# Performance work log

Hardware: AMD Instinct MI355X
Metric: run time of the kernel (lower is better)

## Reference

```python
import jax, jax.numpy as jnp
import numpy as np
import math

H = 1e-4  # finite-difference step
TW = math.pi / 8.0  # transition width
LOW = math.pi / 2.0 - TW
HIGH = math.pi / 2.0 + TW


def _smooth_step(t):
    # equivalent to torch smooth_step with masks: 0 below LOW, 1 above HIGH,
    x = jnp.clip((t - LOW) / (HIGH - LOW), 0.0, 1.0)
    return x * x * (3.0 - 2.0 * x)


def _compute_potential(xyz, a_param, b_param, direction):
    # xyz: [B,3]
    a = jnp.clip(a_param, 0.0, 20.0)
    b = jnp.clip(b_param, 0.0, 20.0)
    r2 = jnp.sum(xyz * xyz, axis=1)          # [B]
    r = jnp.sqrt(r2)
    origin = r == 0.0
    safe_r = jnp.where(origin, 1.0, r)
    p_hat = xyz / safe_r[:, None]            # [B,3]
    dot = p_hat @ direction                  # [B]
    theta = jnp.arccos(jnp.clip(dot, -1.0, 1.0))
    w = _smooth_step(theta)
    # w*direct + (1-w)*ray = 0.5*a*r^2 + (1-w)*0.5*b*r^2*theta^2
    pot = 0.5 * a * r2 + (1.0 - w) * 0.5 * b * r2 * theta * theta
    return jnp.where(origin, 0.0, pot)


def setup_inputs() -> dict:
    key = jax.random.key(0)
    B = 8388608
    xyz = jax.random.normal(key, (B, 3), dtype=jnp.float32)
    theta_dir, phi_dir = 1.0471975511965976, 0.7853981633974483
    direction = jnp.array([
        math.sin(theta_dir) * math.cos(phi_dir),
        math.sin(theta_dir) * math.sin(phi_dir),
        math.cos(theta_dir),
    ], dtype=jnp.float32)
    a_param = jnp.float32(1.0)
    b_param = jnp.float32(10.0)
    return {"xyz": xyz, "a_param": a_param, "b_param": b_param, "direction": direction}


def reference(xyz, a_param, b_param, direction):
    # compute_velocity: central finite differences of the potential, negated
    eye = jnp.eye(3, dtype=xyz.dtype)
    grads = []
    for i in range(3):  # fixed tiny loop over xyz axes
        u_plus = _compute_potential(xyz + H * eye[i], a_param, b_param, direction)
        u_minus = _compute_potential(xyz - H * eye[i], a_param, b_param, direction)
        grads.append((u_plus - u_minus) / (2.0 * H))
    velocity = -jnp.stack(grads, axis=1)  # [B,3]
    return velocity
```

## Files before the change

kernel.cpp:

```cpp
#include <hip/hip_runtime.h>
#include <math.h>

#define HF 1e-4f

#define LOW_F  1.1780972450961724f
#define INV_TW 1.2732395447351628f

__device__ __forceinline__ float fast_acos(float x) {
    float s = __builtin_fabsf(x);
    bool big = s > 0.5f;
    float z = big ? fmaf(-0.5f, s, 0.5f) : x * x;
    float r = big ? __builtin_amdgcn_sqrtf(z) : s;
    float p = fmaf(z, 4.2163199048e-2f, 2.4181311049e-2f);
    p = fmaf(z, p, 4.5470025998e-2f);
    p = fmaf(z, p, 7.4953002686e-2f);
    p = fmaf(z, p, 1.6666752422e-1f);
    float asn = fmaf(r * z, p, r);
    float t2 = 2.0f * asn;
    float rb = (x >= 0.0f) ? t2 : (3.14159274f - t2);
    float rs = (x >= 0.0f) ? (1.57079637f - asn) : (1.57079637f + asn);
    return big ? rb : rs;
}

__device__ __forceinline__ float pot_eval(float x, float y, float z,
                                          float halfa, float halfb,
                                          float dx, float dy, float dz) {
    float r2 = x * x + y * y + z * z;
    float r = __builtin_amdgcn_sqrtf(r2);
    float invr = __builtin_amdgcn_rcpf(r);
    float dot = (x * dx + y * dy + z * dz) * invr;
    dot = fminf(fmaxf(dot, -1.0f), 1.0f);
    float theta = fast_acos(dot);
    float t = (theta - LOW_F) * INV_TW;
    t = fminf(fmaxf(t, 0.0f), 1.0f);
    float w = t * t * (3.0f - 2.0f * t);
    float pot = halfa * r2 + (1.0f - w) * halfb * r2 * theta * theta;
    return (r2 == 0.0f) ? 0.0f : pot;
}

__device__ __forceinline__ void point_velocity(float x, float y, float z,
                                               float halfa, float halfb,
                                               float dx, float dy, float dz,
                                               float& vx, float& vy, float& vz) {
    const float inv2H = 1.0f / 2e-4f;
    float upx = pot_eval(x + HF, y, z, halfa, halfb, dx, dy, dz);
    float umx = pot_eval(x - HF, y, z, halfa, halfb, dx, dy, dz);
    float upy = pot_eval(x, y + HF, z, halfa, halfb, dx, dy, dz);
    float umy = pot_eval(x, y - HF, z, halfa, halfb, dx, dy, dz);
    float upz = pot_eval(x, y, z + HF, halfa, halfb, dx, dy, dz);
    float umz = pot_eval(x, y, z - HF, halfa, halfb, dx, dy, dz);
    vx = -(upx - umx) * inv2H;
    vy = -(upy - umy) * inv2H;
    vz = -(upz - umz) * inv2H;
}

extern "C" __global__ void __launch_bounds__(256)
canyon3d_fd_kernel(const float* __restrict__ xyz,
                   const float* __restrict__ a_param,
                   const float* __restrict__ b_param,
                   const float* __restrict__ dir,
                   float* __restrict__ out,
                   int B) {
    int t = blockIdx.x * blockDim.x + threadIdx.x;
    int base = t * 4;
    if (base >= B) return;

    float a = fminf(fmaxf(a_param[0], 0.0f), 20.0f);
    float b = fminf(fmaxf(b_param[0], 0.0f), 20.0f);
    float halfa = 0.5f * a;
    float halfb = 0.5f * b;
    float dx = dir[0], dy = dir[1], dz = dir[2];

    if (base + 4 <= B) {
        const float4* in4 = (const float4*)xyz;
        float4 A  = in4[3 * t + 0];
        float4 Bv = in4[3 * t + 1];
        float4 C  = in4[3 * t + 2];

        float o0, o1, o2, o3, o4, o5, o6, o7, o8, o9, o10, o11;
        point_velocity(A.x, A.y, A.z,  halfa, halfb, dx, dy, dz, o0, o1, o2);
        point_velocity(A.w, Bv.x, Bv.y, halfa, halfb, dx, dy, dz, o3, o4, o5);
        point_velocity(Bv.z, Bv.w, C.x, halfa, halfb, dx, dy, dz, o6, o7, o8);
        point_velocity(C.y, C.z, C.w,  halfa, halfb, dx, dy, dz, o9, o10, o11);

        float4* out4 = (float4*)out;
        out4[3 * t + 0] = make_float4(o0, o1, o2, o3);
        out4[3 * t + 1] = make_float4(o4, o5, o6, o7);
        out4[3 * t + 2] = make_float4(o8, o9, o10, o11);
    } else {
        for (int i = base; i < B; ++i) {
            float x = xyz[3 * i], y = xyz[3 * i + 1], z = xyz[3 * i + 2];
            float vx, vy, vz;
            point_velocity(x, y, z, halfa, halfb, dx, dy, dz, vx, vy, vz);
            out[3 * i] = vx; out[3 * i + 1] = vy; out[3 * i + 2] = vz;
        }
    }
}

extern "C" void kernel_launch(void* const* d_in, const int* in_sizes, int n_in,
                              void* d_out, int out_size, void* d_ws, size_t ws_size,
                              hipStream_t stream) {
    const float* xyz = (const float*)d_in[0];
    const float* a_param = (const float*)d_in[1];
    const float* b_param = (const float*)d_in[2];
    const float* dir = (const float*)d_in[3];
    float* out = (float*)d_out;

    int B = in_sizes[0] / 3;
    int nthreads = (B + 3) / 4;
    dim3 block(256);
    dim3 grid((nthreads + 255) / 256);
    canyon3d_fd_kernel<<<grid, block, 0, stream>>>(xyz, a_param, b_param, dir, out, B);
}
```

Before: 185.1 us.

## Replace finite-difference potential evaluations with closed-form analytic gradient

Computes the velocity as the exact analytic gradient of the potential instead of six central finite-difference evaluations per point. This removes five of six sqrt/rcp/acos evaluations per point, cutting ALU work so the kernel can approach the memory bound. The result differs slightly from the finite-difference reference, and a clamped reciprocal of sin(theta) guards the pole singularity, which risks accuracy mismatch near dot=±1.

```diff
diff --git a/kernel.cpp b/kernel.cpp
--- a/kernel.cpp
+++ b/kernel.cpp
@@ -1,10 +1,9 @@
 #include <hip/hip_runtime.h>
 #include <math.h>
 
-#define HF 1e-4f
-
-#define LOW_F  1.1780972450961724f
-#define INV_TW 1.2732395447351628f
+#define LOW_F   1.1780972450961724f
+#define INV_TW  1.2732395447351628f
+#define WP_K    7.639437268410977f
 
 __device__ __forceinline__ float fast_acos(float x) {
     float s = __builtin_fabsf(x);
@@ -22,53 +21,60 @@
     return big ? rb : rs;
 }
 
-__device__ __forceinline__ float pot_eval(float x, float y, float z,
-                                          float halfa, float halfb,
-                                          float dx, float dy, float dz) {
+__device__ __forceinline__ void point_velocity(float x, float y, float z,
+                                               float a, float b,
+                                               float dx, float dy, float dz,
+                                               float& vx, float& vy, float& vz) {
     float r2 = x * x + y * y + z * z;
     float r = __builtin_amdgcn_sqrtf(r2);
     float invr = __builtin_amdgcn_rcpf(r);
     float dot = (x * dx + y * dy + z * dz) * invr;
     dot = fminf(fmaxf(dot, -1.0f), 1.0f);
     float theta = fast_acos(dot);
+
     float t = (theta - LOW_F) * INV_TW;
     t = fminf(fmaxf(t, 0.0f), 1.0f);
     float w = t * t * (3.0f - 2.0f * t);
-    float pot = halfa * r2 + (1.0f - w) * halfb * r2 * theta * theta;
-    return (r2 == 0.0f) ? 0.0f : pot;
-}
+    float one_m_w = 1.0f - w;
+    float wp = WP_K * t * (1.0f - t);
 
-__device__ __forceinline__ void point_velocity(float x, float y, float z,
-                                               float halfa, float halfb,
-                                               float dx, float dy, float dz,
-                                               float& vx, float& vy, float& vz) {
-    const float inv2H = 1.0f / 2e-4f;
-    float upx = pot_eval(x + HF, y, z, halfa, halfb, dx, dy, dz);
-    float umx = pot_eval(x - HF, y, z, halfa, halfb, dx, dy, dz);
-    float upy = pot_eval(x, y + HF, z, halfa, halfb, dx, dy, dz);
-    float umy = pot_eval(x, y - HF, z, halfa, halfb, dx, dy, dz);
-    float upz = pot_eval(x, y, z + HF, halfa, halfb, dx, dy, dz);
-    float umz = pot_eval(x, y, z - HF, halfa, halfb, dx, dy, dz);
-    vx = -(upx - umx) * inv2H;
-    vy = -(upy - umy) * inv2H;
-    vz = -(upz - umz) * inv2H;
+    float th2 = theta * theta;
+    float k1 = fmaf(b * th2, one_m_w, a);
+
+    float sin2 = fmaf(-dot, dot, 1.0f);
+    float sinth = __builtin_amdgcn_sqrtf(fmaxf(sin2, 0.0f));
+    float rcpsin = __builtin_amdgcn_rcpf(fmaxf(sinth, 1e-30f));
+    float num = fmaf(2.0f * theta, one_m_w, -th2 * wp);
+    float k2 = (r * 0.5f * b) * num * rcpsin;
+
+    float m = dot * invr;
+    float gx = fmaf(-m, x, dx);
+    float gy = fmaf(-m, y, dy);
+    float gz = fmaf(-m, z, dz);
+
+    float ovx = fmaf(-k1, x, k2 * gx);
+    float ovy = fmaf(-k1, y, k2 * gy);
+    float ovz = fmaf(-k1, z, k2 * gz);
+
+    bool origin = (r2 == 0.0f);
+    vx = origin ? 0.0f : ovx;
+    vy = origin ? 0.0f : ovy;
+    vz = origin ? 0.0f : ovz;
 }
 
 extern "C" __global__ void __launch_bounds__(256)
-canyon3d_fd_kernel(const float* __restrict__ xyz,
-                   const float* __restrict__ a_param,
-                   const float* __restrict__ b_param,
-                   const float* __restrict__ dir,
-                   float* __restrict__ out,
-                   int B) {
+canyon3d_grad_kernel(const float* __restrict__ xyz,
+                     const float* __restrict__ a_param,
+                     const float* __restrict__ b_param,
+                     const float* __restrict__ dir,
+                     float* __restrict__ out,
+                     int B) {
     int t = blockIdx.x * blockDim.x + threadIdx.x;
     int base = t * 4;
     if (base >= B) return;
 
     float a = fminf(fmaxf(a_param[0], 0.0f), 20.0f);
     float b = fminf(fmaxf(b_param[0], 0.0f), 20.0f);
-    float halfa = 0.5f * a;
-    float halfb = 0.5f * b;
     float dx = dir[0], dy = dir[1], dz = dir[2];
 
     if (base + 4 <= B) {
@@ -78,10 +84,10 @@
         float4 C  = in4[3 * t + 2];
 
         float o0, o1, o2, o3, o4, o5, o6, o7, o8, o9, o10, o11;
-        point_velocity(A.x, A.y, A.z,  halfa, halfb, dx, dy, dz, o0, o1, o2);
-        point_velocity(A.w, Bv.x, Bv.y, halfa, halfb, dx, dy, dz, o3, o4, o5);
-        point_velocity(Bv.z, Bv.w, C.x, halfa, halfb, dx, dy, dz, o6, o7, o8);
-        point_velocity(C.y, C.z, C.w,  halfa, halfb, dx, dy, dz, o9, o10, o11);
+        point_velocity(A.x, A.y, A.z,   a, b, dx, dy, dz, o0, o1, o2);
+        point_velocity(A.w, Bv.x, Bv.y, a, b, dx, dy, dz, o3, o4, o5);
+        point_velocity(Bv.z, Bv.w, C.x, a, b, dx, dy, dz, o6, o7, o8);
+        point_velocity(C.y, C.z, C.w,   a, b, dx, dy, dz, o9, o10, o11);
 
         float4* out4 = (float4*)out;
         out4[3 * t + 0] = make_float4(o0, o1, o2, o3);
@@ -91,7 +97,7 @@
         for (int i = base; i < B; ++i) {
             float x = xyz[3 * i], y = xyz[3 * i + 1], z = xyz[3 * i + 2];
             float vx, vy, vz;
-            point_velocity(x, y, z, halfa, halfb, dx, dy, dz, vx, vy, vz);
+            point_velocity(x, y, z, a, b, dx, dy, dz, vx, vy, vz);
             out[3 * i] = vx; out[3 * i + 1] = vy; out[3 * i + 2] = vz;
         }
     }
@@ -110,5 +116,5 @@
     int nthreads = (B + 3) / 4;
     dim3 block(256);
     dim3 grid((nthreads + 255) / 256);
-    canyon3d_fd_kernel<<<grid, block, 0, stream>>>(xyz, a_param, b_param, dir, out, B);
+    canyon3d_grad_kernel<<<grid, block, 0, stream>>>(xyz, a_param, b_param, dir, out, B);
 }
```

After: 184.8 us. No clear change (-0.2%).
